# Optimization experiments

Hardware: AMD Instinct MI355X
Metric: run time of the kernel (lower is better)

## Reference

```python
import jax, jax.numpy as jnp
import numpy as np

EPS = 1e-5  # BatchNorm eps (torch default)
K = 16      # num_neighbors


def _bn(x, gamma, beta, axes):
    # training-mode BatchNorm (biased variance), channel axis = 1
    mu = x.mean(axes, keepdims=True)
    var = x.var(axes, keepdims=True)
    shp = [1] * x.ndim
    shp[1] = -1
    return (x - mu) * jax.lax.rsqrt(var + EPS) * gamma.reshape(shp) + beta.reshape(shp)


def setup_inputs() -> dict:
    key = jax.random.key(0)
    ks = jax.random.split(key, 6)
    B, C, N, E = 4, 3, 4096, 256
    s = lambda k_, shp, fan: jax.random.normal(k_, shp, jnp.float32) * np.float32(1.0 / np.sqrt(fan))
    return {
        "x": jax.random.normal(ks[0], (B, C, N), jnp.float32),
        "g1": jnp.ones((C,), jnp.float32), "b1": jnp.zeros((C,), jnp.float32),
        "W1": s(ks[1], (E, C), C), "bw1": jnp.zeros((E,), jnp.float32),
        "g2a": jnp.ones((C,), jnp.float32), "b2a": jnp.zeros((C,), jnp.float32),
        "W2a": s(ks[2], (E, C), C),
        "g2b": jnp.ones((E,), jnp.float32), "b2b": jnp.zeros((E,), jnp.float32),
        "W2b": s(ks[3], (E, E), E),
        "Wf": s(ks[4], (E, 2 * E), 2 * E), "bf": jnp.zeros((E,), jnp.float32),
    }


def reference(x, g1, b1, W1, bw1, g2a, b2a, W2a, g2b, b2b, W2b, Wf, bf):
    B, C, N = x.shape
    xn = _bn(x, g1, b1, (0, 2))                               # BatchNorm1d
    point_emb = jnp.einsum('ec,bcn->ben', W1, xn) + bw1[None, :, None]  # conv1 (1x1)
    # dist = -||xi - xj||; torch topk(dist, largest=False) picks the K LARGEST
    # distances. Squared distance is monotone in the norm, so top_k on d2 gives
    # identical indices without materializing [B,3,N,N].
    x2 = jnp.sum(xn * xn, axis=1)                             # [B,N]
    d2 = x2[:, :, None] + x2[:, None, :] - 2.0 * jnp.einsum('bcn,bcm->bnm', xn, xn)
    _, idx = jax.lax.top_k(d2, min(K, N))                     # [B,N,K]
    idx = idx[:, :, 1:]                                       # original loop skips index 0
    gathered = jax.vmap(lambda xb, ib: xb[:, ib])(xn, idx)    # [B,C,N,K-1]
    neigh = gathered - xn[:, :, :, None]                      # edge features
    h = _bn(neigh, g2a, b2a, (0, 2, 3))                       # BatchNorm2d(Cin)
    h = jnp.einsum('ec,bcnk->benk', W2a, h)                   # 1x1 conv, no bias
    h = jax.nn.gelu(_bn(h, g2b, b2b, (0, 2, 3)), approximate=False)
    h = jnp.einsum('fe,benk->bfnk', W2b, h)                   # 1x1 conv, no bias
    neigh_emb = h.max(-1)                                     # max over neighbors
    feat = jnp.concatenate([point_emb, neigh_emb], axis=1)    # [B,2E,N]
    return jnp.einsum('of,bfn->bon', Wf, feat) + bf[None, :, None]
```

## Files before the change

### kernel.cpp

```cpp
#include <hip/hip_runtime.h>
#include <float.h>
#include <math.h>

#define EPS 1e-5f
constexpr int B = 4, C = 3, N = 4096, E = 256;
constexpr int KNN = 15;
constexpr int BN_ = B * N;
constexpr int P = 8;
constexpr int SR  = 264;
constexpr int SRF = 520;

typedef short bf8 __attribute__((ext_vector_type(8)));
typedef float f4  __attribute__((ext_vector_type(4)));

static __device__ __forceinline__ unsigned short f2bf(float f) {
    union { float f; unsigned int u; } v; v.f = f;
    unsigned int r = v.u + 0x7FFFu + ((v.u >> 16) & 1u);
    return (unsigned short)(r >> 16);
}
static __device__ __forceinline__ bf8 ld_bf8(const unsigned short* p) {
    return *(const bf8*)p;
}
static __device__ __forceinline__ float gelu_t(float v) {
    float z = v * fmaf(v * v, 0.07135482f, 1.59576912f);
    float r = __builtin_amdgcn_rcpf(1.f + __expf(z));
    return fmaf(-v, r, v);
}

__global__ void __launch_bounds__(256) compute_xn_cvt(
        const float* __restrict__ x,
        const float* __restrict__ g1, const float* __restrict__ b1,
        float4* __restrict__ xn4,
        const float* __restrict__ W2b, const float* __restrict__ Wf,
        unsigned short* __restrict__ w2b_t, unsigned short* __restrict__ wf_t,
        float* __restrict__ S9) {
    int blk = blockIdx.x;
    int t = threadIdx.x;
    if (blk < 64) {
        __shared__ float red[256][6];
        float s[3] = {0.f, 0.f, 0.f}, ss[3] = {0.f, 0.f, 0.f};
        #pragma unroll
        for (int c = 0; c < 3; c++) {
            for (int i4 = t; i4 < BN_ / 4; i4 += 256) {
                int b = i4 >> 10, n4 = i4 & 1023;
                float4 v = ((const float4*)(x + (b * C + c) * N))[n4];
                s[c]  += v.x + v.y + v.z + v.w;
                ss[c] += v.x * v.x + v.y * v.y + v.z * v.z + v.w * v.w;
            }
        }
        #pragma unroll
        for (int c = 0; c < 3; c++) { red[t][c] = s[c]; red[t][3 + c] = ss[c]; }
        __syncthreads();
        for (int w = 128; w > 0; w >>= 1) {
            if (t < w) {
                #pragma unroll
                for (int j = 0; j < 6; j++) red[t][j] += red[t + w][j];
            }
            __syncthreads();
        }
        float mu[3], rs[3];
        #pragma unroll
        for (int c = 0; c < 3; c++) {
            mu[c] = red[0][c] / (float)BN_;
            float var = red[0][3 + c] / (float)BN_ - mu[c] * mu[c];
            rs[c] = rsqrtf(var + EPS);
        }
        int i = blk * 256 + t;
        int b = i >> 12, n = i & (N - 1);
        float v[3];
        #pragma unroll
        for (int c = 0; c < C; c++)
            v[c] = (x[(b * C + c) * N + n] - mu[c]) * rs[c] * g1[c] + b1[c];
        float4 o; o.x = v[0]; o.y = v[1]; o.z = v[2];
        o.w = v[0] * v[0] + v[1] * v[1] + v[2] * v[2];
        xn4[i] = o;
        return;
    }
    if (blk == 64) {
        for (int j = t; j < 64 * 9; j += 256) S9[j] = 0.f;
    }
    int ch = (blk - 64) * 256 + t;
    if (ch < 8192) {
        int lane = ch & 63, kb = (ch >> 6) & 7, ft16 = ch >> 9;
        int row = ft16 * 16 + (lane & 15);
        int col = kb * 32 + (lane >> 4) * 8;
        #pragma unroll
        for (int j = 0; j < 8; j++)
            w2b_t[ch * 8 + j] = f2bf(W2b[row * 256 + col + j]);
    } else {
        int c2 = ch - 8192;
        int lane = c2 & 63, kb = (c2 >> 6) & 15, ot = c2 >> 10;
        int row = ot * 16 + (lane & 15);
        int col = kb * 32 + (lane >> 4) * 8;
        #pragma unroll
        for (int j = 0; j < 8; j++)
            wf_t[c2 * 8 + j] = f2bf(Wf[row * 512 + col + j]);
    }
}

__global__ void __launch_bounds__(256, 4) knn_kernel(const float4* __restrict__ xn4,
                                                     unsigned short* __restrict__ idxout,
                                                     float* __restrict__ S9) {
    __shared__ float smom[4][15][9];
    int w = threadIdx.x >> 6, lane = threadIdx.x & 63;
    int i = blockIdx.x * 4 + w;
    int b = i >> 12, n = i & (N - 1);
    const float4* xb = xn4 + b * N;
    float4 qv = xb[n];
    float d[64];
    #pragma unroll
    for (int s = 0; s < 64; s++) {
        float4 p = xb[s * 64 + lane];
        d[s] = qv.w + p.w - 2.f * (qv.x * p.x + qv.y * p.y + qv.z * p.z);
    }
    float cm[8];
    #pragma unroll
    for (int c = 0; c < 8; c++) {
        float v = d[c * 8];
        #pragma unroll
        for (int s = 1; s < 8; s++) v = fmaxf(v, d[c * 8 + s]);
        cm[c] = v;
    }
    float bv = cm[0];
    #pragma unroll
    for (int c = 1; c < 8; c++) bv = fmaxf(bv, cm[c]);

    int myj = 0;
    for (int r = 0; r < 16; r++) {
        float wv = bv;
        #pragma unroll
        for (int off = 32; off > 0; off >>= 1)
            wv = fmaxf(wv, __shfl_xor(wv, off));
        unsigned long long msk = __ballot(bv == wv);
        int wl = __ffsll(msk) - 1;
        int gi = 0;
        if (lane == wl) {
            int cstar = 0; bool got = false;
            #pragma unroll
            for (int c = 0; c < 8; c++) {
                bool h = !got && (cm[c] == bv);
                cstar = h ? c : cstar;
                got = got || h;
            }
            int slot = 0;
            #pragma unroll
            for (int c = 0; c < 8; c++) {
                if (c == cstar) {
                    bool g2 = false;
                    #pragma unroll
                    for (int s = 0; s < 8; s++) {
                        bool h = !g2 && (d[c * 8 + s] == bv);
                        slot = h ? (c * 8 + s) : slot;
                        g2 = g2 || h;
                    }
                    #pragma unroll
                    for (int s = 0; s < 8; s++)
                        d[c * 8 + s] = (c * 8 + s == slot) ? -FLT_MAX : d[c * 8 + s];
                    float v = d[c * 8];
                    #pragma unroll
                    for (int s = 1; s < 8; s++) v = fmaxf(v, d[c * 8 + s]);
                    cm[c] = v;
                }
            }
            bv = cm[0];
            #pragma unroll
            for (int c = 1; c < 8; c++) bv = fmaxf(bv, cm[c]);
            gi = slot * 64 + lane;
        }
        int g = __shfl(gi, wl);
        if (lane == r - 1) myj = g;
    }

    bool act = lane < 15;
    if (act) idxout[i * KNN + lane] = (unsigned short)myj;
    float4 pj = xb[act ? myj : n];
    float v0 = pj.x - qv.x, v1 = pj.y - qv.y, v2 = pj.z - qv.z;
    if (act) {
        float* mm = smom[w][lane];
        mm[0] = v0; mm[1] = v1; mm[2] = v2;
        mm[3] = v0 * v0; mm[4] = v1 * v1; mm[5] = v2 * v2;
        mm[6] = v0 * v1; mm[7] = v0 * v2; mm[8] = v1 * v2;
    }
    __syncthreads();
    int t = threadIdx.x;
    if (t < 36) {
        int wsel = t / 9, j = t % 9;
        float a = 0.f;
        #pragma unroll
        for (int u = 0; u < 15; u++) a += smom[wsel][u][j];
        atomicAdd(&S9[((blockIdx.x * 4 + wsel) & 63) * 9 + j], a);
    }
}

__global__ void __launch_bounds__(512, 4) fused_final(
        const float4* __restrict__ xn4, const unsigned short* __restrict__ idx,
        const float* __restrict__ S9,
        const float* __restrict__ g2a, const float* __restrict__ b2a,
        const float* __restrict__ W2a,
        const float* __restrict__ g2b, const float* __restrict__ b2b,
        const unsigned short* __restrict__ w2b_t,
        const float* __restrict__ W1, const float* __restrict__ bw1,
        const unsigned short* __restrict__ wf_t, const float* __restrict__ bfv,
        float* __restrict__ out) {
    __shared__ __align__(16) unsigned short hh_bf[128 * SR];
    __shared__ __align__(16) unsigned short feat_bf[8 * SRF];
    __shared__ __align__(16) float4 hhat4[P][16];
    __shared__ float falpha[3], fbeta[3], fmu[3], fEhh[3][3];
    int i0 = blockIdx.x * P;
    int t = threadIdx.x;
    int b = i0 >> 12, n0 = i0 & (N - 1);
    const float4* xb = xn4 + b * N;
    const float cnt = (float)(BN_ * KNN);

    if (t < 64) {
        float v[9];
        #pragma unroll
        for (int j = 0; j < 9; j++) v[j] = S9[t * 9 + j];
        #pragma unroll
        for (int off = 32; off > 0; off >>= 1)
            #pragma unroll
            for (int j = 0; j < 9; j++) v[j] += __shfl_xor(v[j], off);
        if (t == 0) {
            float s2[3][3];
            s2[0][0] = v[3]; s2[1][1] = v[4]; s2[2][2] = v[5];
            s2[0][1] = s2[1][0] = v[6]; s2[0][2] = s2[2][0] = v[7]; s2[1][2] = s2[2][1] = v[8];
            float al[3], be[3], m[3];
            #pragma unroll
            for (int c = 0; c < 3; c++) {
                m[c] = v[c] / cnt;
                float var = s2[c][c] / cnt - m[c] * m[c];
                al[c] = g2a[c] * rsqrtf(var + EPS);
                be[c] = b2a[c] - m[c] * al[c];
                falpha[c] = al[c]; fbeta[c] = be[c]; fmu[c] = m[c];
            }
            #pragma unroll
            for (int c = 0; c < 3; c++)
                #pragma unroll
                for (int cc = 0; cc < 3; cc++)
                    fEhh[c][cc] = al[c] * al[cc] * (s2[c][cc] / cnt)
                                + al[c] * be[cc] * m[c] + be[c] * al[cc] * m[cc] + be[c] * be[cc];
        }
    }
    __syncthreads();

    float4 w4;
    {
        int e = t & 255;
        float wv0 = W2a[e * 3], wv1 = W2a[e * 3 + 1], wv2 = W2a[e * 3 + 2];
        float Eh0 = falpha[0] * fmu[0] + fbeta[0];
        float Eh1 = falpha[1] * fmu[1] + fbeta[1];
        float Eh2 = falpha[2] * fmu[2] + fbeta[2];
        float mean = wv0 * Eh0 + wv1 * Eh1 + wv2 * Eh2;
        float m2 = wv0 * (wv0 * fEhh[0][0] + wv1 * fEhh[0][1] + wv2 * fEhh[0][2])
                 + wv1 * (wv0 * fEhh[1][0] + wv1 * fEhh[1][1] + wv2 * fEhh[1][2])
                 + wv2 * (wv0 * fEhh[2][0] + wv1 * fEhh[2][1] + wv2 * fEhh[2][2]);
        float var = m2 - mean * mean;
        float s = g2b[e] * rsqrtf(var + EPS);
        w4.x = wv0 * s; w4.y = wv1 * s; w4.z = wv2 * s; w4.w = b2b[e] - mean * s;
    }

    if (t < P * KNN) {
        int p = t / KNN, k = t % KNN;
        int j = idx[(i0 + p) * KNN + k];
        float4 pj = xb[j];
        float4 pn = xb[n0 + p];
        float4 h;
        h.x = falpha[0] * (pj.x - pn.x) + fbeta[0];
        h.y = falpha[1] * (pj.y - pn.y) + fbeta[1];
        h.z = falpha[2] * (pj.z - pn.z) + fbeta[2];
        h.w = 0.f;
        hhat4[p][k] = h;
    }
    __syncthreads();

    {
        int e = t & 255;
        int ph = t >> 8;
        #pragma unroll
        for (int pp = 0; pp < 4; pp++) {
            int p = ph * 4 + pp;
            float g0 = 0.f;
            #pragma unroll
            for (int k = 0; k < KNN; k++) {
                float4 hv = hhat4[p][k];
                float v = fmaf(w4.x, hv.x, fmaf(w4.y, hv.y, fmaf(w4.z, hv.z, w4.w)));
                float g = gelu_t(v);
                hh_bf[(16 * p + k) * SR + e] = f2bf(g);
                if (k == 0) g0 = g;
            }
            hh_bf[(16 * p + 15) * SR + e] = f2bf(g0);
            float4 pv = xb[n0 + p];
            feat_bf[p * SRF + e] = f2bf(bw1[e] + W1[e * 3] * pv.x
                       + W1[e * 3 + 1] * pv.y + W1[e * 3 + 2] * pv.z);
        }
    }
    __syncthreads();

    int w = t >> 6, lane = t & 63;
    int m = lane & 15, q = lane >> 4;

    {
        #pragma unroll
        for (int f = 0; f < 2; f++) {
            int ft = w * 2 + f;
            bf8 a[8];
            #pragma unroll
            for (int kb = 0; kb < 8; kb++)
                a[kb] = ld_bf8(w2b_t + ft * 4096 + kb * 512 + lane * 8);
            #pragma unroll 1
            for (int pr = 0; pr < 4; pr++) {
                bf8 hfr[2][8];
                #pragma unroll
                for (int pi = 0; pi < 2; pi++)
                    #pragma unroll
                    for (int kb = 0; kb < 8; kb++)
                        hfr[pi][kb] = ld_bf8(&hh_bf[(16 * (pr * 2 + pi) + m) * SR + kb * 32 + q * 8]);
                #pragma unroll
                for (int pi = 0; pi < 2; pi++) {
                    f4 acc = {0.f, 0.f, 0.f, 0.f};
                    #pragma unroll
                    for (int kb = 0; kb < 8; kb++)
                        acc = __builtin_amdgcn_mfma_f32_16x16x32_bf16(hfr[pi][kb], a[kb], acc, 0, 0, 0);
                    float mx = fmaxf(fmaxf(acc[0], acc[1]), fmaxf(acc[2], acc[3]));
                    mx = fmaxf(mx, __shfl_xor(mx, 16));
                    mx = fmaxf(mx, __shfl_xor(mx, 32));
                    if (lane < 16)
                        feat_bf[(pr * 2 + pi) * SRF + E + ft * 16 + lane] = f2bf(mx);
                }
            }
        }
    }
    __syncthreads();

    {
        bf8 fb[16];
        #pragma unroll
        for (int kb = 0; kb < 16; kb++)
            fb[kb] = ld_bf8(&feat_bf[(m & 7) * SRF + kb * 32 + q * 8]);
        #pragma unroll
        for (int o2 = 0; o2 < 2; o2++) {
            int ot = w * 2 + o2;
            f4 acc = {0.f, 0.f, 0.f, 0.f};
            #pragma unroll
            for (int kb = 0; kb < 16; kb++) {
                bf8 a = ld_bf8(wf_t + ot * 8192 + kb * 512 + lane * 8);
                acc = __builtin_amdgcn_mfma_f32_16x16x32_bf16(a, fb[kb], acc, 0, 0, 0);
            }
            if (m < P) {
                int o0 = ot * 16 + 4 * q;
                out[(b * E + o0 + 0) * N + n0 + m] = acc[0] + bfv[o0 + 0];
                out[(b * E + o0 + 1) * N + n0 + m] = acc[1] + bfv[o0 + 1];
                out[(b * E + o0 + 2) * N + n0 + m] = acc[2] + bfv[o0 + 2];
                out[(b * E + o0 + 3) * N + n0 + m] = acc[3] + bfv[o0 + 3];
            }
        }
    }
}

extern "C" void kernel_launch(void* const* d_in, const int* in_sizes, int n_in,
                              void* d_out, int out_size, void* d_ws, size_t ws_size,
                              hipStream_t stream) {
    (void)in_sizes; (void)n_in; (void)out_size; (void)ws_size;
    const float* x   = (const float*)d_in[0];
    const float* g1  = (const float*)d_in[1];
    const float* b1  = (const float*)d_in[2];
    const float* W1  = (const float*)d_in[3];
    const float* bw1 = (const float*)d_in[4];
    const float* g2a = (const float*)d_in[5];
    const float* b2a = (const float*)d_in[6];
    const float* W2a = (const float*)d_in[7];
    const float* g2b = (const float*)d_in[8];
    const float* b2b = (const float*)d_in[9];
    const float* W2b = (const float*)d_in[10];
    const float* Wf  = (const float*)d_in[11];
    const float* bfv = (const float*)d_in[12];
    float* out = (float*)d_out;

    char* ws = (char*)d_ws;
    size_t off = 0;
    auto alloc = [&](size_t bytes) { size_t o = off; off = (off + bytes + 255) & ~(size_t)255; return o; };
    float4* xn4           = (float4*)(ws + alloc(sizeof(float4) * BN_));
    unsigned short* idx   = (unsigned short*)(ws + alloc(sizeof(unsigned short) * BN_ * KNN));
    float* S9             = (float*)(ws + alloc(sizeof(float) * 64 * 9));
    unsigned short* w2bt  = (unsigned short*)(ws + alloc(sizeof(unsigned short) * E * E));
    unsigned short* wft   = (unsigned short*)(ws + alloc(sizeof(unsigned short) * E * 2 * E));

    compute_xn_cvt<<<160, 256, 0, stream>>>(x, g1, b1, xn4, W2b, Wf, w2bt, wft, S9);
    knn_kernel<<<BN_ / 4, 256, 0, stream>>>(xn4, idx, S9);
    fused_final<<<BN_ / P, 512, 0, stream>>>(xn4, idx, S9, g2a, b2a, W2a, g2b, b2b,
                                             w2bt, W1, bw1, wft, bfv, out);
}
```

Baseline: 254.8 us.

## Rewrite kNN top-k as threshold selection and reorder MFMA loop for fragment reuse

```diff
diff --git a/kernel.cpp b/kernel.cpp
--- a/kernel.cpp
+++ b/kernel.cpp
@@ -102,11 +102,13 @@
                                                      unsigned short* __restrict__ idxout,
                                                      float* __restrict__ S9) {
     __shared__ float smom[4][15][9];
+    __shared__ int   sidx[4][16];
     int w = threadIdx.x >> 6, lane = threadIdx.x & 63;
     int i = blockIdx.x * 4 + w;
     int b = i >> 12, n = i & (N - 1);
     const float4* xb = xn4 + b * N;
     float4 qv = xb[n];
+    if (lane < 16) sidx[w][lane] = n;
     float d[64];
     #pragma unroll
     for (int s = 0; s < 64; s++) {
@@ -125,57 +127,48 @@
     #pragma unroll
     for (int c = 1; c < 8; c++) bv = fmaxf(bv, cm[c]);
 
-    int myj = 0;
+    float wvs[16];
+    #pragma unroll
     for (int r = 0; r < 16; r++) {
         float wv = bv;
         #pragma unroll
         for (int off = 32; off > 0; off >>= 1)
             wv = fmaxf(wv, __shfl_xor(wv, off));
-        unsigned long long msk = __ballot(bv == wv);
-        int wl = __ffsll(msk) - 1;
-        int gi = 0;
-        if (lane == wl) {
-            int cstar = 0; bool got = false;
+        wvs[r] = wv;
+        if (r < 15 && bv == wv) {
+            float nb = -FLT_MAX;
             #pragma unroll
             for (int c = 0; c < 8; c++) {
-                bool h = !got && (cm[c] == bv);
-                cstar = h ? c : cstar;
-                got = got || h;
-            }
-            int slot = 0;
-            #pragma unroll
-            for (int c = 0; c < 8; c++) {
-                if (c == cstar) {
-                    bool g2 = false;
+                if (cm[c] >= wv) {
+                    float v = -FLT_MAX;
                     #pragma unroll
                     for (int s = 0; s < 8; s++) {
-                        bool h = !g2 && (d[c * 8 + s] == bv);
-                        slot = h ? (c * 8 + s) : slot;
-                        g2 = g2 || h;
+                        float xv = d[c * 8 + s];
+                        v = (xv < wv) ? fmaxf(v, xv) : v;
                     }
-                    #pragma unroll
-                    for (int s = 0; s < 8; s++)
-                        d[c * 8 + s] = (c * 8 + s == slot) ? -FLT_MAX : d[c * 8 + s];
-                    float v = d[c * 8];
-                    #pragma unroll
-                    for (int s = 1; s < 8; s++) v = fmaxf(v, d[c * 8 + s]);
                     cm[c] = v;
                 }
-            }
-            bv = cm[0];
-            #pragma unroll
-            for (int c = 1; c < 8; c++) bv = fmaxf(bv, cm[c]);
-            gi = slot * 64 + lane;
-        }
-        int g = __shfl(gi, wl);
-        if (lane == r - 1) myj = g;
-    }
-
-    bool act = lane < 15;
-    if (act) idxout[i * KNN + lane] = (unsigned short)myj;
-    float4 pj = xb[act ? myj : n];
-    float v0 = pj.x - qv.x, v1 = pj.y - qv.y, v2 = pj.z - qv.z;
-    if (act) {
+                nb = fmaxf(nb, cm[c]);
+            }
+            bv = nb;
+        }
+    }
+    float thr = wvs[15];
+    #pragma unroll
+    for (int s = 0; s < 64; s++) {
+        float v = d[s];
+        if (v >= thr) {
+            int rank = 0;
+            #pragma unroll
+            for (int j = 0; j < 15; j++) rank += (v < wvs[j]) ? 1 : 0;
+            if (rank > 0) sidx[w][rank - 1] = s * 64 + lane;
+        }
+    }
+    if (lane < 15) {
+        int j = sidx[w][lane];
+        idxout[i * KNN + lane] = (unsigned short)j;
+        float4 pj = xb[j];
+        float v0 = pj.x - qv.x, v1 = pj.y - qv.y, v2 = pj.z - qv.z;
         float* mm = smom[w][lane];
         mm[0] = v0; mm[1] = v1; mm[2] = v2;
         mm[3] = v0 * v0; mm[4] = v1 * v1; mm[5] = v2 * v2;
@@ -300,33 +293,29 @@
     int m = lane & 15, q = lane >> 4;
 
     {
-        #pragma unroll
-        for (int f = 0; f < 2; f++) {
-            int ft = w * 2 + f;
-            bf8 a[8];
+        bf8 a2[2][8];
+        #pragma unroll
+        for (int f = 0; f < 2; f++)
             #pragma unroll
             for (int kb = 0; kb < 8; kb++)
-                a[kb] = ld_bf8(w2b_t + ft * 4096 + kb * 512 + lane * 8);
-            #pragma unroll 1
-            for (int pr = 0; pr < 4; pr++) {
-                bf8 hfr[2][8];
+                a2[f][kb] = ld_bf8(w2b_t + (w * 2 + f) * 4096 + kb * 512 + lane * 8);
+        #pragma unroll 1
+        for (int p8 = 0; p8 < 8; p8++) {
+            bf8 hfr[8];
+            #pragma unroll
+            for (int kb = 0; kb < 8; kb++)
+                hfr[kb] = ld_bf8(&hh_bf[(16 * p8 + m) * SR + kb * 32 + q * 8]);
+            #pragma unroll
+            for (int f = 0; f < 2; f++) {
+                f4 acc = {0.f, 0.f, 0.f, 0.f};
                 #pragma unroll
-                for (int pi = 0; pi < 2; pi++)
-                    #pragma unroll
-                    for (int kb = 0; kb < 8; kb++)
-                        hfr[pi][kb] = ld_bf8(&hh_bf[(16 * (pr * 2 + pi) + m) * SR + kb * 32 + q * 8]);
-                #pragma unroll
-                for (int pi = 0; pi < 2; pi++) {
-                    f4 acc = {0.f, 0.f, 0.f, 0.f};
-                    #pragma unroll
-                    for (int kb = 0; kb < 8; kb++)
-                        acc = __builtin_amdgcn_mfma_f32_16x16x32_bf16(hfr[pi][kb], a[kb], acc, 0, 0, 0);
-                    float mx = fmaxf(fmaxf(acc[0], acc[1]), fmaxf(acc[2], acc[3]));
-                    mx = fmaxf(mx, __shfl_xor(mx, 16));
-                    mx = fmaxf(mx, __shfl_xor(mx, 32));
-                    if (lane < 16)
-                        feat_bf[(pr * 2 + pi) * SRF + E + ft * 16 + lane] = f2bf(mx);
-                }
+                for (int kb = 0; kb < 8; kb++)
+                    acc = __builtin_amdgcn_mfma_f32_16x16x32_bf16(hfr[kb], a2[f][kb], acc, 0, 0, 0);
+                float mx = fmaxf(fmaxf(acc[0], acc[1]), fmaxf(acc[2], acc[3]));
+                mx = fmaxf(mx, __shfl_xor(mx, 16));
+                mx = fmaxf(mx, __shfl_xor(mx, 32));
+                if (lane < 16)
+                    feat_bf[p8 * SRF + E + (w * 2 + f) * 16 + lane] = f2bf(mx);
             }
         }
     }
```

New measurement: 262.3 us. 2.9% more time.
